# Optimization experiments

Measured on AMD Instinct MI355X. Metric: run time of the kernel, lower is better.

Reference implementation:

```python
import jax, jax.numpy as jnp
import numpy as np

IN_CH = 8      # in_channels
CIN = 80       # cin_channels (mel)
DI_BASE = 2
POS_GROUP = 4
NCH = 256      # n_channels
NLAYERS = 8
K = 3          # kernel_size
B = 1          # spect batch; audio batch = B * POS_GROUP
T = 4096
C2L = 2 * NCH * NLAYERS


def _conv1x1(x, w, b):
    # x: [B, C, T], w: [O, C], b: [O]
    return jnp.einsum('bct,oc->bot', x, w) + b[None, :, None]


def _dilated_conv(x, w, b, dilation):
    # x: [B, C, T], w: [O, C, K], 'same' padding as in torch Conv1d
    pad = dilation * (K - 1) // 2
    y = jax.lax.conv_general_dilated(
        x, w, window_strides=(1,), padding=[(pad, pad)],
        rhs_dilation=(dilation,), dimension_numbers=('NCH', 'OIH', 'NCH'))
    return y + b[None, :, None]


def setup_inputs() -> dict:
    key = jax.random.key(0)
    ks = jax.random.split(key, 12)
    s = 0.05
    d = {}
    d['audio'] = jax.random.normal(ks[0], (B * POS_GROUP, IN_CH, T), jnp.float32)
    d['spect'] = jax.random.normal(ks[1], (B, CIN, T), jnp.float32)
    d['pos'] = jax.random.randint(ks[2], (B * POS_GROUP,), 0, POS_GROUP)
    d['start_w'] = jax.random.normal(ks[3], (NCH, IN_CH), jnp.float32) * s
    d['start_b'] = jnp.zeros((NCH,), jnp.float32)
    d['cond_w'] = jax.random.normal(ks[4], (C2L, CIN), jnp.float32) * s
    d['cond_b'] = jnp.zeros((C2L,), jnp.float32)
    d['pos_emb_w'] = jax.random.normal(ks[5], (POS_GROUP, 128), jnp.float32) * s
    d['pos_lin_w'] = jax.random.normal(ks[6], (C2L, 128), jnp.float32) * s
    d['pos_lin_b'] = jnp.zeros((C2L,), jnp.float32)
    d['in_w'] = jax.random.normal(ks[7], (NLAYERS, 2 * NCH, NCH, K), jnp.float32) * s
    d['in_b'] = jnp.zeros((NLAYERS, 2 * NCH), jnp.float32)
    d['rs_w'] = jax.random.normal(ks[8], (NLAYERS - 1, 2 * NCH, NCH), jnp.float32) * s
    d['rs_b'] = jnp.zeros((NLAYERS - 1, 2 * NCH), jnp.float32)
    d['rs_last_w'] = jax.random.normal(ks[9], (NCH, NCH), jnp.float32) * s
    d['rs_last_b'] = jnp.zeros((NCH,), jnp.float32)
    d['end_w'] = jax.random.normal(ks[10], (2 * IN_CH, NCH), jnp.float32) * s
    d['end_b'] = jnp.zeros((2 * IN_CH,), jnp.float32)
    return d


def reference(audio, spect, pos, start_w, start_b, cond_w, cond_b,
              pos_emb_w, pos_lin_w, pos_lin_b, in_w, in_b,
              rs_w, rs_b, rs_last_w, rs_last_b, end_w, end_b):
    h = _conv1x1(audio, start_w, start_b)               # [BG, NCH, T]
    out = jnp.zeros_like(h)
    cond = _conv1x1(spect, cond_w, cond_b)              # [B, 2*NCH*L, T]
    # repeat(1, pos_group, 1).view(-1, C, T) == consecutive batch tiling
    cond = jnp.repeat(cond, POS_GROUP, axis=0)          # [BG, 2*NCH*L, T]
    pe = jax.nn.relu(pos_emb_w[pos])                    # [BG, 128]
    pc = (pe @ pos_lin_w.T + pos_lin_b)[:, :, None]     # [BG, 2*NCH*L, 1]
    for i in range(NLAYERS):
        off = i * 2 * NCH
        in_act = (_dilated_conv(h, in_w[i], in_b[i], DI_BASE ** i)
                  + cond[:, off:off + 2 * NCH]
                  + pc[:, off:off + 2 * NCH])
        acts = jnp.tanh(in_act[:, :NCH]) * jax.nn.sigmoid(in_act[:, NCH:])
        if i < NLAYERS - 1:
            rs = _conv1x1(acts, rs_w[i], rs_b[i])       # [BG, 2*NCH, T]
            h = h + rs[:, :NCH]
            out = out + rs[:, NCH:]
        else:
            out = out + _conv1x1(acts, rs_last_w, rs_last_b)
    y = _conv1x1(out, end_w, end_b)                     # [BG, 2*IN_CH, T]
    return y[:, :IN_CH], y[:, IN_CH:]
```

## Files before the change

kernel.cpp:

```cpp
#include <hip/hip_runtime.h>
#include <stdint.h>

#define T_LEN 4096
#define PAD   128
#define HROWS (T_LEN + 2*PAD)
#define NCH   256
#define M2    512
#define BG    4
#define NL    8

using f4  = __attribute__((ext_vector_type(4))) float;
using bh8 = __attribute__((ext_vector_type(8))) short;
using s4v = __attribute__((ext_vector_type(4))) short;
using u4  = __attribute__((ext_vector_type(4))) unsigned int;

static __device__ __forceinline__ short f2b(float f){
  unsigned u = __builtin_bit_cast(unsigned, f);
  unsigned r = (u + 0x7FFFu + ((u >> 16) & 1u)) >> 16;
  return (short)r;
}
static __device__ __forceinline__ float b2f(short s){
  unsigned u = ((unsigned)(unsigned short)s) << 16;
  return __builtin_bit_cast(float, u);
}

#define MFMA(a,b,c) __builtin_amdgcn_mfma_f32_16x16x32_bf16((a),(b),(c),0,0,0)


#define PAD_BLK0 1024
#define E_BLK0   1280
#define ST_BLK0  1408
#define CB_BLK0  1536
#define H0_BLK0  1600
#define ALL_BLKS 1856

__global__ __launch_bounds__(256) void prep_all(
    const float* __restrict__ audio, const float* __restrict__ spect,
    const int* __restrict__ pos, const float* __restrict__ start_w,
    const float* __restrict__ start_b, const float* __restrict__ cond_w,
    const float* __restrict__ cond_b, const float* __restrict__ pos_emb_w,
    const float* __restrict__ pos_lin_w, const float* __restrict__ pos_lin_b,
    const float* __restrict__ in_w, const float* __restrict__ in_b,
    const float* __restrict__ rs_w, const float* __restrict__ rs_b,
    const float* __restrict__ rs_last_w, const float* __restrict__ rs_last_b,
    const float* __restrict__ end_w, const float* __restrict__ end_b,
    short* __restrict__ W1, short* __restrict__ W2, short* __restrict__ Wcn,
    float* __restrict__ rsb8, short* __restrict__ hA, short* __restrict__ hB,
    short* __restrict__ Es, float* __restrict__ ebl, short* __restrict__ spectT,
    float* __restrict__ cb){
  __shared__ float smem[4224];
  const int bid = blockIdx.x, tid = threadIdx.x;

  if (bid < PAD_BLK0){
    const int n1 = NL*3*8*8*4*512;
    const int n2 = NL*8*8*2*512;
    const int n4 = NL*8*4*4*512;
    const int n3 = NL*M2;
    for (int i = bid*256 + tid; i < n1+n2+n4+n3; i += 1024*256){
      if (i < n1){
        int j = i & 7, lane = (i >> 3) & 63, f = (i >> 9) & 3, kk = (i >> 11) & 7, w = (i >> 14) & 7;
        int lt = i >> 17;
        int tap = lt % 3, l = lt / 3;
        int o = (f < 2) ? (w*32 + f*16 + (lane & 15)) : (256 + w*32 + (f-2)*16 + (lane & 15));
        int c = kk*32 + (lane >> 4)*8 + j;
        W1[i] = f2b(in_w[(((l*M2 + o)*NCH + c)*3) + tap]);
      } else if (i < n1+n2){
        int q = i - n1;
        int j = q & 7, lane = (q >> 3) & 63, f = (q >> 9) & 1, kk = (q >> 10) & 7, w = (q >> 13) & 7;
        int l = q >> 16;
        int o = w*32 + f*16 + (lane & 15);
        int c = kk*32 + (lane >> 4)*8 + j;
        W2[q] = (l < 7) ? f2b(rs_w[((size_t)(l*M2 + o))*NCH + c]) : (short)0;
      } else if (i < n1+n2+n4){
        int r = i - n1 - n2;
        int j = r & 7, lane = (r >> 3) & 63, f = (r >> 9) & 3, kk = (r >> 11) & 3, w = (r >> 13) & 7;
        int l = r >> 16;
        int o = (f < 2) ? (w*32 + f*16 + (lane & 15)) : (256 + w*32 + (f-2)*16 + (lane & 15));
        int k = kk*32 + (lane >> 4)*8 + j;
        Wcn[r] = (k < 80) ? f2b(cond_w[(size_t)(l*M2 + o)*80 + k]) : (short)0;
      } else {
        int k = i - n1 - n2 - n4;
        int o = k & 511, l = k >> 9;
        rsb8[k] = (l < 7) ? rs_b[l*M2 + o] : 0.f;
      }
    }
  } else if (bid < E_BLK0){
    int i = (bid - PAD_BLK0)*256 + tid;
    short* h = (i < 32768) ? hA : hB;
    int j = (i & 32767) << 3;
    int b = j >> 16;
    int r = j & 65535;
    int row = r >> 8, c = r & 255;
    int grow = (row < PAD) ? row : (T_LEN + PAD + (row - PAD));
    *(u4*)(h + ((size_t)b*HROWS + grow)*NCH + c) = (u4){0,0,0,0};
  } else if (bid < ST_BLK0){
    float* ew_s = smem; float* red = smem + 256;
    int e = bid - E_BLK0;
    const int l = e >> 4, o = e & 15;
    const int c = tid;
    ew_s[c] = end_w[o*256 + c];
    __syncthreads();
    const float* Wsrc = (l < 7) ? (rs_w + ((size_t)(l*M2 + NCH))*NCH) : rs_last_w;
    float acc = 0.f;
    #pragma unroll 8
    for (int cp = 0; cp < 256; ++cp)
      acc += ew_s[cp] * Wsrc[(size_t)cp*NCH + c];
    int kk = c >> 5, g = (c >> 3) & 3, j = c & 7;
    Es[(((size_t)l*8 + kk)*64 + g*16 + o)*8 + j] = f2b(acc);
    float bv = (l < 7) ? rs_b[l*M2 + NCH + c] : rs_last_b[c];
    red[c] = ew_s[c] * bv;
    __syncthreads();
    for (int s = 128; s > 0; s >>= 1){
      if (c < s) red[c] += red[c + s];
      __syncthreads();
    }
    if (c == 0) ebl[l*16 + o] = red[0] + ((l == 0) ? end_b[o] : 0.f);
  } else if (bid < CB_BLK0){
    float (*tile)[65] = (float(*)[65])smem;
    int e = bid - ST_BLK0;
    int t0 = (e & 63)*64, k0 = (e >> 6)*64;
    for (int i = tid; i < 64*64; i += 256){
      int kr = i >> 6, tt = i & 63;
      int k = k0 + kr;
      tile[kr][tt] = (k < 80) ? spect[(size_t)k*T_LEN + t0 + tt] : 0.f;
    }
    __syncthreads();
    for (int i = tid; i < 64*64; i += 256){
      int r = i >> 6, kk = i & 63;
      spectT[(size_t)(t0 + r)*128 + k0 + kk] = f2b(tile[kk][r]);
    }
  } else if (bid < H0_BLK0){
    int e = bid - CB_BLK0;
    int b = e >> 4;
    int ch = (e & 15)*256 + tid;
    int p = pos[b];
    float acc = pos_lin_b[ch] + in_b[ch] + cond_b[ch];
    for (int k = 0; k < 128; ++k){
      float ev = pos_emb_w[p*128 + k];
      ev = ev > 0.f ? ev : 0.f;
      acc += ev * pos_lin_w[ch*128 + k];
    }
    cb[b*4096 + ch] = acc;
  } else {
    float* sw = smem; float* sb = smem + 2048;
    int e = bid - H0_BLK0;
    int b = e >> 6, t0 = (e & 63)*64;
    for (int i = tid; i < NCH*8; i += 256) sw[i] = start_w[i];
    for (int i = tid; i < NCH;   i += 256) sb[i] = start_b[i];
    __syncthreads();
    int t = t0 + (tid & 63);
    int cg = tid >> 6;
    float av[8];
    #pragma unroll
    for (int ic = 0; ic < 8; ++ic) av[ic] = audio[((size_t)(b*8 + ic))*T_LEN + t];
    short* dst = hA + ((size_t)b*HROWS + PAD + t)*NCH;
    for (int c = cg*64; c < cg*64 + 64; ++c){
      float acc = sb[c];
      #pragma unroll
      for (int ic = 0; ic < 8; ++ic) acc += sw[c*8 + ic]*av[ic];
      dst[c] = f2b(acc);
    }
  }
}

__global__ __launch_bounds__(512, 2) void wn_layer(
    const short* __restrict__ hSrc, short* __restrict__ hDst,
    const short* __restrict__ W1l, const short* __restrict__ W2l,
    const short* __restrict__ Wcl, const short* __restrict__ Esl,
    const short* __restrict__ spectTp,
    const float* __restrict__ cb_l, const float* __restrict__ rsb_l,
    const float* __restrict__ ebl_l, float* __restrict__ yacc,
    int dil, int flags){

  __shared__ short Ht[3*64*NCH];
  __shared__ short xb[64*NCH];
  __shared__ short St[64*128];

  const int tid  = threadIdx.x;
  const int w    = tid >> 6, lane = tid & 63;
  const int l15  = lane & 15, g = lane >> 4;
  const int tile = blockIdx.x, b = blockIdx.y;
  const int sw8  = (l15 & 7) << 3;
  const bool first = flags & 1, last = flags & 2;

  f4 acc[4][4];
  #pragma unroll
  for (int f = 0; f < 4; ++f)
    #pragma unroll
    for (int nf = 0; nf < 4; ++nf) acc[f][nf] = (f4){0.f,0.f,0.f,0.f};

  bh8 Ap[3][4], Bp[3][4];

#define LAc(S, BUF) do{ const short* _p = Wcl + w*8192 + (S)*2048 + lane*8; \
    Ap[BUF][0]=*(const bh8*)(_p);      Ap[BUF][1]=*(const bh8*)(_p+512); \
    Ap[BUF][2]=*(const bh8*)(_p+1024); Ap[BUF][3]=*(const bh8*)(_p+1536); }while(0)
#define LBc(S, BUF) do{ const int _c=((S)*32+g*8)^sw8; \
    Bp[BUF][0]=*(const bh8*)(St + ( 0+l15)*128 + _c); \
    Bp[BUF][1]=*(const bh8*)(St + (16+l15)*128 + _c); \
    Bp[BUF][2]=*(const bh8*)(St + (32+l15)*128 + _c); \
    Bp[BUF][3]=*(const bh8*)(St + (48+l15)*128 + _c); }while(0)
#define LA1(S, BUF) do{ const int _tap=(S)>>3, _kk=(S)&7; \
    const short* _p = W1l + _tap*131072 + w*16384 + _kk*2048 + lane*8; \
    Ap[BUF][0]=*(const bh8*)(_p);      Ap[BUF][1]=*(const bh8*)(_p+512); \
    Ap[BUF][2]=*(const bh8*)(_p+1024); Ap[BUF][3]=*(const bh8*)(_p+1536); }while(0)
#define LB1(S, BUF) do{ const int _tap=(S)>>3, _kk=(S)&7; const int _c=(_kk*32+g*8)^sw8; \
    Bp[BUF][0]=*(const bh8*)(Ht + _tap*16384 + ( 0+l15)*NCH + _c); \
    Bp[BUF][1]=*(const bh8*)(Ht + _tap*16384 + (16+l15)*NCH + _c); \
    Bp[BUF][2]=*(const bh8*)(Ht + _tap*16384 + (32+l15)*NCH + _c); \
    Bp[BUF][3]=*(const bh8*)(Ht + _tap*16384 + (48+l15)*NCH + _c); }while(0)
#define LAX(S, BUF) do{ if((S)<3) LAc((S),BUF); else LA1((S)-3,BUF); }while(0)
#define LBX(S, BUF) do{ if((S)<3) LBc((S),BUF); else LB1((S)-3,BUF); }while(0)
#define LA2(S, BUF) do{ \
    const short* _p = W2l + w*8192 + (S)*1024 + lane*8; \
    Ap[BUF][0]=*(const bh8*)(_p);      Ap[BUF][1]=*(const bh8*)(_p+512); }while(0)
#define LB2(S, BUF) do{ const int _c=((S)*32+g*8)^sw8; \
    Bp[BUF][0]=*(const bh8*)(xb + ( 0+l15)*NCH + _c); \
    Bp[BUF][1]=*(const bh8*)(xb + (16+l15)*NCH + _c); \
    Bp[BUF][2]=*(const bh8*)(xb + (32+l15)*NCH + _c); \
    Bp[BUF][3]=*(const bh8*)(xb + (48+l15)*NCH + _c); }while(0)

  LAX(0, 0);

  {
    const int rsub = tid >> 5;
    const int innr = (tid & 31) << 3;
    #pragma unroll
    for (int tap = 0; tap < 3; ++tap){
      const int gbase = b*HROWS + PAD + tile*64 + (tap-1)*dil;
      #pragma unroll
      for (int ch = 0; ch < 4; ++ch){
        int r = ch*16 + rsub;
        u4 v = *(const u4*)(hSrc + (size_t)(gbase + r)*NCH + innr);
        *(u4*)(Ht + tap*16384 + r*NCH + (innr ^ ((r & 7) << 3))) = v;
      }
    }
    #pragma unroll
    for (int s = 0; s < 2; ++s){
      int id = tid + s*512;
      int r = id >> 4, c8 = (id & 15) << 3;
      u4 v = *(const u4*)(spectTp + (size_t)(tile*64 + r)*128 + c8);
      *(u4*)(St + r*128 + (c8 ^ ((r & 7) << 3))) = v;
    }
  }
  __syncthreads();

  LBX(0, 0);
  LAX(1, 1); LBX(1, 1);
  #pragma unroll
  for (int s = 0; s < 27; ++s){
    const int cur = s % 3, pf = (s+2) % 3;
    if (s < 25){ LAX(s+2, pf); LBX(s+2, pf); }
    #pragma unroll
    for (int f = 0; f < 4; ++f)
      #pragma unroll
      for (int nf = 0; nf < 4; ++nf)
        acc[f][nf] = MFMA(Ap[cur][f], Bp[cur][nf], acc[f][nf]);
  }

  float bias[4][4];
  #pragma unroll
  for (int f = 0; f < 4; ++f){
    int ch = ((f < 2) ? (w*32 + f*16) : (256 + w*32 + (f-2)*16)) + 4*g;
    f4 t = *(const f4*)(cb_l + b*4096 + ch);
    #pragma unroll
    for (int j = 0; j < 4; ++j) bias[f][j] = t[j];
  }
  float rbv[2][4];
  #pragma unroll
  for (int f = 0; f < 2; ++f){
    f4 t = *(const f4*)(rsb_l + w*32 + f*16 + 4*g);
    #pragma unroll
    for (int j = 0; j < 4; ++j) rbv[f][j] = t[j];
  }

  #pragma unroll
  for (int f = 0; f < 2; ++f){
    #pragma unroll
    for (int nf = 0; nf < 4; ++nf){
      int tl = nf*16 + l15;
      s4v pk;
      #pragma unroll
      for (int j = 0; j < 4; ++j){
        float xl = acc[f][nf][j]   + bias[f][j];
        float xh = acc[f+2][nf][j] + bias[f+2][j];
        xl = fminf(fmaxf(xl, -30.f), 30.f);
        xh = fminf(fmaxf(xh, -30.f), 30.f);
        float e2 = __expf(2.f*xl);
        float th = (e2 - 1.f)/(e2 + 1.f);
        float sg = 1.f/(1.f + __expf(-xh));
        pk[j] = f2b(th * sg);
      }
      *(s4v*)(xb + tl*NCH + ((w*32 + f*16 + 4*g) ^ sw8)) = pk;
    }
  }
  if (!last) LA2(0, 0);
  __syncthreads();

  if (!last){
    #pragma unroll
    for (int f = 0; f < 2; ++f)
      #pragma unroll
      for (int nf = 0; nf < 4; ++nf) acc[f][nf] = (f4){0.f,0.f,0.f,0.f};
    LB2(0, 0);
    #pragma unroll
    for (int s = 0; s < 8; ++s){
      const int cur = s & 1, nxt = cur ^ 1;
      if (s < 7){ LA2(s+1, nxt); LB2(s+1, nxt); }
      #pragma unroll
      for (int f = 0; f < 2; ++f)
        #pragma unroll
        for (int nf = 0; nf < 4; ++nf)
          acc[f][nf] = MFMA(Ap[cur][f], Bp[cur][nf], acc[f][nf]);
    }
    #pragma unroll
    for (int f = 0; f < 2; ++f){
      #pragma unroll
      for (int nf = 0; nf < 4; ++nf){
        int tl = nf*16 + l15;
        int cb0 = w*32 + f*16 + 4*g;
        s4v hold = *(const s4v*)(Ht + 16384 + tl*NCH + (cb0 ^ sw8));
        s4v pk;
        #pragma unroll
        for (int j = 0; j < 4; ++j)
          pk[j] = f2b(b2f(hold[j]) + acc[f][nf][j] + rbv[f][j]);
        *(s4v*)(hDst + ((size_t)b*HROWS + PAD + tile*64 + tl)*NCH + cb0) = pk;
      }
    }
  }
  {
    const int nfq = w & 3, kh = w >> 2;
    f4 ya = (f4){0.f,0.f,0.f,0.f};
    #pragma unroll
    for (int s = 0; s < 4; ++s){
      int kks = kh*4 + s;
      bh8 av = *(const bh8*)(Esl + ((size_t)kks*64 + lane)*8);
      bh8 bv = *(const bh8*)(xb + (nfq*16 + l15)*NCH + ((kks*32 + g*8) ^ sw8));
      ya = MFMA(av, bv, ya);
    }
    float* yp = yacc + (((size_t)(b*T_LEN + tile*64 + nfq*16 + l15))*2 + kh)*16 + g*4;
    f4 prev = first ? (f4){0.f,0.f,0.f,0.f} : *(const f4*)yp;
    f4 o;
    #pragma unroll
    for (int j = 0; j < 4; ++j)
      o[j] = prev[j] + ya[j] + ((kh == 0) ? ebl_l[g*4 + j] : 0.f);
    *(f4*)yp = o;
  }
#undef LAc
#undef LBc
#undef LA1
#undef LB1
#undef LAX
#undef LBX
#undef LA2
#undef LB2
}

__global__ void final_y(const float* __restrict__ yacc, float* __restrict__ y){
  __shared__ float tl[16][65];
  int b = blockIdx.y, t0 = blockIdx.x*64;
  int i = threadIdx.x;
  #pragma unroll
  for (int s = 0; s < 4; ++s){
    int idx = i + s*256;
    int t = idx >> 4, o = idx & 15;
    size_t base = ((size_t)(b*T_LEN + t0 + t))*32 + o;
    tl[o][t] = yacc[base] + yacc[base + 16];
  }
  __syncthreads();
  #pragma unroll
  for (int s = 0; s < 4; ++s){
    int idx = i + s*256;
    int o = idx >> 6, t = idx & 63;
    float v = tl[o][t];
    float* dst = (o < 8) ? (y + ((size_t)(b*8 + o))*T_LEN)
                         : (y + 131072 + ((size_t)(b*8 + o - 8))*T_LEN);
    dst[t0 + t] = v;
  }
}

extern "C" void kernel_launch(void* const* d_in, const int* in_sizes, int n_in,
                              void* d_out, int out_size, void* d_ws, size_t ws_size,
                              hipStream_t stream){
  const float* audio      = (const float*)d_in[0];
  const float* spect      = (const float*)d_in[1];
  const int*   pos        = (const int*)  d_in[2];
  const float* start_w    = (const float*)d_in[3];
  const float* start_b    = (const float*)d_in[4];
  const float* cond_w     = (const float*)d_in[5];
  const float* cond_b     = (const float*)d_in[6];
  const float* pos_emb_w  = (const float*)d_in[7];
  const float* pos_lin_w  = (const float*)d_in[8];
  const float* pos_lin_b  = (const float*)d_in[9];
  const float* in_w       = (const float*)d_in[10];
  const float* in_b       = (const float*)d_in[11];
  const float* rs_w       = (const float*)d_in[12];
  const float* rs_b       = (const float*)d_in[13];
  const float* rs_last_w  = (const float*)d_in[14];
  const float* rs_last_b  = (const float*)d_in[15];
  const float* end_w      = (const float*)d_in[16];
  const float* end_b      = (const float*)d_in[17];
  float* y = (float*)d_out;

  char* ws = (char*)d_ws;
  size_t off = 0;
  auto alloc = [&](size_t bytes) -> void* {
    void* p = ws + off;
    off += (bytes + 255) & ~(size_t)255;
    return p;
  };
  const size_t hBytes = (size_t)BG*HROWS*NCH*2;
  short* hA     = (short*)alloc(hBytes);
  short* hB     = (short*)alloc(hBytes);
  short* W1     = (short*)alloc((size_t)NL*3*8*8*4*512*2);
  short* W2     = (short*)alloc((size_t)NL*8*8*2*512*2);
  short* Wcn    = (short*)alloc((size_t)NL*8*4*4*512*2);
  float* rsb8   = (float*)alloc((size_t)NL*M2*4);
  float* cb     = (float*)alloc((size_t)BG*4096*4);
  short* spectT = (short*)alloc((size_t)4096*128*2);
  short* Es     = (short*)alloc((size_t)NL*8*64*8*2);
  float* ebl    = (float*)alloc((size_t)NL*16*4);
  float* yacc   = (float*)alloc((size_t)BG*T_LEN*2*16*4);
  if (off > ws_size) return;

  prep_all<<<ALL_BLKS, 256, 0, stream>>>(
      audio, spect, pos, start_w, start_b, cond_w, cond_b, pos_emb_w, pos_lin_w,
      pos_lin_b, in_w, in_b, rs_w, rs_b, rs_last_w, rs_last_b, end_w, end_b,
      W1, W2, Wcn, rsb8, hA, hB, Es, ebl, spectT, cb);

  for (int l = 0; l < NL; ++l){
    const short* hS = (l & 1) ? hB : hA;
    short*       hD = (l & 1) ? hA : hB;
    int flags = (l == 0 ? 1 : 0) | (l == NL-1 ? 2 : 0);
    wn_layer<<<dim3(64, BG), 512, 0, stream>>>(
        hS, hD,
        W1 + (size_t)l*3*131072,
        W2 + (size_t)l*65536,
        Wcn + (size_t)l*65536,
        Es + (size_t)l*4096,
        spectT,
        cb + l*M2,
        rsb8 + l*M2,
        ebl + l*16,
        yacc, 1 << l, flags);
  }
  final_y<<<dim3(64, BG), 256, 0, stream>>>(yacc, y);
}
```

Before: 219.6 us.

## Split wn_layer work across 16 waves with 1024-thread blocks

Each layer block now runs 16 waves instead of 8, and each wave owns 16 output channels (tanh and sigmoid halves) instead of 32. The weight pre-swizzle in prep_all, the register tiles, the prefetch pipeline, the residual GEMM and the end-projection partial sums (now four k-slices in yacc) are all re-laid out to match. The aim is more wave-level parallelism and latency hiding per CU, given only 256 blocks. In exchange the smaller per-wave tile means less operand reuse, and 1024-thread blocks allow at most one block per CU.

New measurement: 233.1 us. 6.2% more time.

```diff
diff --git a/kernel.cpp b/kernel.cpp
--- a/kernel.cpp
+++ b/kernel.cpp
@@ -52,30 +52,30 @@
   const int bid = blockIdx.x, tid = threadIdx.x;
 
   if (bid < PAD_BLK0){
-    const int n1 = NL*3*8*8*4*512;
-    const int n2 = NL*8*8*2*512;
-    const int n4 = NL*8*4*4*512;
+    const int n1 = NL*3*16*8*2*512;
+    const int n2 = NL*16*8*512;
+    const int n4 = NL*16*4*2*512;
     const int n3 = NL*M2;
     for (int i = bid*256 + tid; i < n1+n2+n4+n3; i += 1024*256){
       if (i < n1){
-        int j = i & 7, lane = (i >> 3) & 63, f = (i >> 9) & 3, kk = (i >> 11) & 7, w = (i >> 14) & 7;
+        int j = i & 7, lane = (i >> 3) & 63, f = (i >> 9) & 1, kk = (i >> 10) & 7, w = (i >> 13) & 15;
         int lt = i >> 17;
         int tap = lt % 3, l = lt / 3;
-        int o = (f < 2) ? (w*32 + f*16 + (lane & 15)) : (256 + w*32 + (f-2)*16 + (lane & 15));
+        int o = (f == 0) ? (w*16 + (lane & 15)) : (256 + w*16 + (lane & 15));
         int c = kk*32 + (lane >> 4)*8 + j;
         W1[i] = f2b(in_w[(((l*M2 + o)*NCH + c)*3) + tap]);
       } else if (i < n1+n2){
         int q = i - n1;
-        int j = q & 7, lane = (q >> 3) & 63, f = (q >> 9) & 1, kk = (q >> 10) & 7, w = (q >> 13) & 7;
+        int j = q & 7, lane = (q >> 3) & 63, kk = (q >> 9) & 7, w = (q >> 12) & 15;
         int l = q >> 16;
-        int o = w*32 + f*16 + (lane & 15);
+        int o = w*16 + (lane & 15);
         int c = kk*32 + (lane >> 4)*8 + j;
         W2[q] = (l < 7) ? f2b(rs_w[((size_t)(l*M2 + o))*NCH + c]) : (short)0;
       } else if (i < n1+n2+n4){
         int r = i - n1 - n2;
-        int j = r & 7, lane = (r >> 3) & 63, f = (r >> 9) & 3, kk = (r >> 11) & 3, w = (r >> 13) & 7;
+        int j = r & 7, lane = (r >> 3) & 63, f = (r >> 9) & 1, kk = (r >> 10) & 3, w = (r >> 12) & 15;
         int l = r >> 16;
-        int o = (f < 2) ? (w*32 + f*16 + (lane & 15)) : (256 + w*32 + (f-2)*16 + (lane & 15));
+        int o = (f == 0) ? (w*16 + (lane & 15)) : (256 + w*16 + (lane & 15));
         int k = kk*32 + (lane >> 4)*8 + j;
         Wcn[r] = (k < 80) ? f2b(cond_w[(size_t)(l*M2 + o)*80 + k]) : (short)0;
       } else {
@@ -163,7 +163,7 @@
   }
 }
 
-__global__ __launch_bounds__(512, 2) void wn_layer(
+__global__ __launch_bounds__(1024) void wn_layer(
     const short* __restrict__ hSrc, short* __restrict__ hDst,
     const short* __restrict__ W1l, const short* __restrict__ W2l,
     const short* __restrict__ Wcl, const short* __restrict__ Esl,
@@ -183,26 +183,24 @@
   const int sw8  = (l15 & 7) << 3;
   const bool first = flags & 1, last = flags & 2;
 
-  f4 acc[4][4];
-  #pragma unroll
-  for (int f = 0; f < 4; ++f)
+  f4 acc[2][4];
+  #pragma unroll
+  for (int f = 0; f < 2; ++f)
     #pragma unroll
     for (int nf = 0; nf < 4; ++nf) acc[f][nf] = (f4){0.f,0.f,0.f,0.f};
 
-  bh8 Ap[3][4], Bp[3][4];
-
-#define LAc(S, BUF) do{ const short* _p = Wcl + w*8192 + (S)*2048 + lane*8; \
-    Ap[BUF][0]=*(const bh8*)(_p);      Ap[BUF][1]=*(const bh8*)(_p+512); \
-    Ap[BUF][2]=*(const bh8*)(_p+1024); Ap[BUF][3]=*(const bh8*)(_p+1536); }while(0)
+  bh8 Ap[3][2], Bp[2][4];
+
+#define LAc(S, BUF) do{ const short* _p = Wcl + w*4096 + (S)*1024 + lane*8; \
+    Ap[BUF][0]=*(const bh8*)(_p); Ap[BUF][1]=*(const bh8*)(_p+512); }while(0)
 #define LBc(S, BUF) do{ const int _c=((S)*32+g*8)^sw8; \
     Bp[BUF][0]=*(const bh8*)(St + ( 0+l15)*128 + _c); \
     Bp[BUF][1]=*(const bh8*)(St + (16+l15)*128 + _c); \
     Bp[BUF][2]=*(const bh8*)(St + (32+l15)*128 + _c); \
     Bp[BUF][3]=*(const bh8*)(St + (48+l15)*128 + _c); }while(0)
 #define LA1(S, BUF) do{ const int _tap=(S)>>3, _kk=(S)&7; \
-    const short* _p = W1l + _tap*131072 + w*16384 + _kk*2048 + lane*8; \
-    Ap[BUF][0]=*(const bh8*)(_p);      Ap[BUF][1]=*(const bh8*)(_p+512); \
-    Ap[BUF][2]=*(const bh8*)(_p+1024); Ap[BUF][3]=*(const bh8*)(_p+1536); }while(0)
+    const short* _p = W1l + _tap*131072 + w*8192 + _kk*1024 + lane*8; \
+    Ap[BUF][0]=*(const bh8*)(_p); Ap[BUF][1]=*(const bh8*)(_p+512); }while(0)
 #define LB1(S, BUF) do{ const int _tap=(S)>>3, _kk=(S)&7; const int _c=(_kk*32+g*8)^sw8; \
     Bp[BUF][0]=*(const bh8*)(Ht + _tap*16384 + ( 0+l15)*NCH + _c); \
     Bp[BUF][1]=*(const bh8*)(Ht + _tap*16384 + (16+l15)*NCH + _c); \
@@ -211,8 +209,8 @@
 #define LAX(S, BUF) do{ if((S)<3) LAc((S),BUF); else LA1((S)-3,BUF); }while(0)
 #define LBX(S, BUF) do{ if((S)<3) LBc((S),BUF); else LB1((S)-3,BUF); }while(0)
 #define LA2(S, BUF) do{ \
-    const short* _p = W2l + w*8192 + (S)*1024 + lane*8; \
-    Ap[BUF][0]=*(const bh8*)(_p);      Ap[BUF][1]=*(const bh8*)(_p+512); }while(0)
+    const short* _p = W2l + w*4096 + (S)*512 + lane*8; \
+    Ap[BUF][0]=*(const bh8*)(_p); }while(0)
 #define LB2(S, BUF) do{ const int _c=((S)*32+g*8)^sw8; \
     Bp[BUF][0]=*(const bh8*)(xb + ( 0+l15)*NCH + _c); \
     Bp[BUF][1]=*(const bh8*)(xb + (16+l15)*NCH + _c); \
@@ -220,24 +218,22 @@
     Bp[BUF][3]=*(const bh8*)(xb + (48+l15)*NCH + _c); }while(0)
 
   LAX(0, 0);
+  LAX(1, 1);
 
   {
-    const int rsub = tid >> 5;
-    const int innr = (tid & 31) << 3;
     #pragma unroll
     for (int tap = 0; tap < 3; ++tap){
       const int gbase = b*HROWS + PAD + tile*64 + (tap-1)*dil;
       #pragma unroll
-      for (int ch = 0; ch < 4; ++ch){
-        int r = ch*16 + rsub;
+      for (int ch = 0; ch < 2; ++ch){
+        int id = tid + ch*1024;
+        int r = id >> 5, innr = (id & 31) << 3;
         u4 v = *(const u4*)(hSrc + (size_t)(gbase + r)*NCH + innr);
         *(u4*)(Ht + tap*16384 + r*NCH + (innr ^ ((r & 7) << 3))) = v;
       }
     }
-    #pragma unroll
-    for (int s = 0; s < 2; ++s){
-      int id = tid + s*512;
-      int r = id >> 4, c8 = (id & 15) << 3;
+    {
+      int r = tid >> 4, c8 = (tid & 15) << 3;
       u4 v = *(const u4*)(spectTp + (size_t)(tile*64 + r)*128 + c8);
       *(u4*)(St + r*128 + (c8 ^ ((r & 7) << 3))) = v;
     }
@@ -245,99 +241,87 @@
   __syncthreads();
 
   LBX(0, 0);
-  LAX(1, 1); LBX(1, 1);
   #pragma unroll
   for (int s = 0; s < 27; ++s){
-    const int cur = s % 3, pf = (s+2) % 3;
-    if (s < 25){ LAX(s+2, pf); LBX(s+2, pf); }
-    #pragma unroll
-    for (int f = 0; f < 4; ++f)
+    const int curA = s % 3, curB = s & 1;
+    if (s < 25) LAX(s+2, (s+2) % 3);
+    if (s < 26) LBX(s+1, curB ^ 1);
+    #pragma unroll
+    for (int f = 0; f < 2; ++f)
       #pragma unroll
       for (int nf = 0; nf < 4; ++nf)
-        acc[f][nf] = MFMA(Ap[cur][f], Bp[cur][nf], acc[f][nf]);
-  }
-
-  float bias[4][4];
-  #pragma unroll
-  for (int f = 0; f < 4; ++f){
-    int ch = ((f < 2) ? (w*32 + f*16) : (256 + w*32 + (f-2)*16)) + 4*g;
-    f4 t = *(const f4*)(cb_l + b*4096 + ch);
+        acc[f][nf] = MFMA(Ap[curA][f], Bp[curB][nf], acc[f][nf]);
+  }
+
+  float bias[2][4];
+  #pragma unroll
+  for (int f = 0; f < 2; ++f){
+    f4 t = *(const f4*)(cb_l + b*4096 + f*256 + w*16 + 4*g);
     #pragma unroll
     for (int j = 0; j < 4; ++j) bias[f][j] = t[j];
   }
-  float rbv[2][4];
-  #pragma unroll
-  for (int f = 0; f < 2; ++f){
-    f4 t = *(const f4*)(rsb_l + w*32 + f*16 + 4*g);
-    #pragma unroll
-    for (int j = 0; j < 4; ++j) rbv[f][j] = t[j];
-  }
-
-  #pragma unroll
-  for (int f = 0; f < 2; ++f){
-    #pragma unroll
-    for (int nf = 0; nf < 4; ++nf){
-      int tl = nf*16 + l15;
-      s4v pk;
-      #pragma unroll
-      for (int j = 0; j < 4; ++j){
-        float xl = acc[f][nf][j]   + bias[f][j];
-        float xh = acc[f+2][nf][j] + bias[f+2][j];
-        xl = fminf(fmaxf(xl, -30.f), 30.f);
-        xh = fminf(fmaxf(xh, -30.f), 30.f);
-        float e2 = __expf(2.f*xl);
-        float th = (e2 - 1.f)/(e2 + 1.f);
-        float sg = 1.f/(1.f + __expf(-xh));
-        pk[j] = f2b(th * sg);
-      }
-      *(s4v*)(xb + tl*NCH + ((w*32 + f*16 + 4*g) ^ sw8)) = pk;
-    }
+  float rbv[4];
+  {
+    f4 t = *(const f4*)(rsb_l + w*16 + 4*g);
+    #pragma unroll
+    for (int j = 0; j < 4; ++j) rbv[j] = t[j];
+  }
+
+  #pragma unroll
+  for (int nf = 0; nf < 4; ++nf){
+    int tl = nf*16 + l15;
+    s4v pk;
+    #pragma unroll
+    for (int j = 0; j < 4; ++j){
+      float xl = acc[0][nf][j] + bias[0][j];
+      float xh = acc[1][nf][j] + bias[1][j];
+      xl = fminf(fmaxf(xl, -30.f), 30.f);
+      xh = fminf(fmaxf(xh, -30.f), 30.f);
+      float e2 = __expf(2.f*xl);
+      float th = (e2 - 1.f)/(e2 + 1.f);
+      float sg = 1.f/(1.f + __expf(-xh));
+      pk[j] = f2b(th * sg);
+    }
+    *(s4v*)(xb + tl*NCH + ((w*16 + 4*g) ^ sw8)) = pk;
   }
   if (!last) LA2(0, 0);
   __syncthreads();
 
   if (!last){
     #pragma unroll
-    for (int f = 0; f < 2; ++f)
-      #pragma unroll
-      for (int nf = 0; nf < 4; ++nf) acc[f][nf] = (f4){0.f,0.f,0.f,0.f};
+    for (int nf = 0; nf < 4; ++nf) acc[0][nf] = (f4){0.f,0.f,0.f,0.f};
     LB2(0, 0);
     #pragma unroll
     for (int s = 0; s < 8; ++s){
       const int cur = s & 1, nxt = cur ^ 1;
       if (s < 7){ LA2(s+1, nxt); LB2(s+1, nxt); }
       #pragma unroll
-      for (int f = 0; f < 2; ++f)
-        #pragma unroll
-        for (int nf = 0; nf < 4; ++nf)
-          acc[f][nf] = MFMA(Ap[cur][f], Bp[cur][nf], acc[f][nf]);
-    }
-    #pragma unroll
-    for (int f = 0; f < 2; ++f){
+      for (int nf = 0; nf < 4; ++nf)
+        acc[0][nf] = MFMA(Ap[cur][0], Bp[cur][nf], acc[0][nf]);
+    }
+    #pragma unroll
+    for (int nf = 0; nf < 4; ++nf){
+      int tl = nf*16 + l15;
+      int cb0 = w*16 + 4*g;
+      s4v hold = *(const s4v*)(Ht + 16384 + tl*NCH + (cb0 ^ sw8));
+      s4v pk;
       #pragma unroll
-      for (int nf = 0; nf < 4; ++nf){
-        int tl = nf*16 + l15;
-        int cb0 = w*32 + f*16 + 4*g;
-        s4v hold = *(const s4v*)(Ht + 16384 + tl*NCH + (cb0 ^ sw8));
-        s4v pk;
-        #pragma unroll
-        for (int j = 0; j < 4; ++j)
-          pk[j] = f2b(b2f(hold[j]) + acc[f][nf][j] + rbv[f][j]);
-        *(s4v*)(hDst + ((size_t)b*HROWS + PAD + tile*64 + tl)*NCH + cb0) = pk;
-      }
+      for (int j = 0; j < 4; ++j)
+        pk[j] = f2b(b2f(hold[j]) + acc[0][nf][j] + rbv[j]);
+      *(s4v*)(hDst + ((size_t)b*HROWS + PAD + tile*64 + tl)*NCH + cb0) = pk;
     }
   }
   {
     const int nfq = w & 3, kh = w >> 2;
     f4 ya = (f4){0.f,0.f,0.f,0.f};
     #pragma unroll
-    for (int s = 0; s < 4; ++s){
-      int kks = kh*4 + s;
+    for (int s = 0; s < 2; ++s){
+      int kks = kh*2 + s;
       bh8 av = *(const bh8*)(Esl + ((size_t)kks*64 + lane)*8);
       bh8 bv = *(const bh8*)(xb + (nfq*16 + l15)*NCH + ((kks*32 + g*8) ^ sw8));
       ya = MFMA(av, bv, ya);
     }
-    float* yp = yacc + (((size_t)(b*T_LEN + tile*64 + nfq*16 + l15))*2 + kh)*16 + g*4;
+    float* yp = yacc + (((size_t)(b*T_LEN + tile*64 + nfq*16 + l15))*4 + kh)*16 + g*4;
     f4 prev = first ? (f4){0.f,0.f,0.f,0.f} : *(const f4*)yp;
     f4 o;
     #pragma unroll
@@ -363,8 +347,8 @@
   for (int s = 0; s < 4; ++s){
     int idx = i + s*256;
     int t = idx >> 4, o = idx & 15;
-    size_t base = ((size_t)(b*T_LEN + t0 + t))*32 + o;
-    tl[o][t] = yacc[base] + yacc[base + 16];
+    size_t base = ((size_t)(b*T_LEN + t0 + t))*64 + o;
+    tl[o][t] = yacc[base] + yacc[base + 16] + yacc[base + 32] + yacc[base + 48];
   }
   __syncthreads();
   #pragma unroll
@@ -411,15 +395,15 @@
   const size_t hBytes = (size_t)BG*HROWS*NCH*2;
   short* hA     = (short*)alloc(hBytes);
   short* hB     = (short*)alloc(hBytes);
-  short* W1     = (short*)alloc((size_t)NL*3*8*8*4*512*2);
-  short* W2     = (short*)alloc((size_t)NL*8*8*2*512*2);
-  short* Wcn    = (short*)alloc((size_t)NL*8*4*4*512*2);
+  short* W1     = (short*)alloc((size_t)NL*3*16*8*2*512*2);
+  short* W2     = (short*)alloc((size_t)NL*16*8*512*2);
+  short* Wcn    = (short*)alloc((size_t)NL*16*4*2*512*2);
   float* rsb8   = (float*)alloc((size_t)NL*M2*4);
   float* cb     = (float*)alloc((size_t)BG*4096*4);
   short* spectT = (short*)alloc((size_t)4096*128*2);
   short* Es     = (short*)alloc((size_t)NL*8*64*8*2);
   float* ebl    = (float*)alloc((size_t)NL*16*4);
-  float* yacc   = (float*)alloc((size_t)BG*T_LEN*2*16*4);
+  float* yacc   = (float*)alloc((size_t)BG*T_LEN*4*16*4);
   if (off > ws_size) return;
 
   prep_all<<<ALL_BLKS, 256, 0, stream>>>(
@@ -431,7 +415,7 @@
     const short* hS = (l & 1) ? hB : hA;
     short*       hD = (l & 1) ? hA : hB;
     int flags = (l == 0 ? 1 : 0) | (l == NL-1 ? 2 : 0);
-    wn_layer<<<dim3(64, BG), 512, 0, stream>>>(
+    wn_layer<<<dim3(64, BG), 1024, 0, stream>>>(
         hS, hD,
         W1 + (size_t)l*3*131072,
         W2 + (size_t)l*65536,
```

## Vectorize weight packing, dedupe dilated-conv halo loads, remap block order

Applied to the files above, without the earlier changes.

The prep kernel now packs eight bf16 weights per thread with vector loads and one 16-byte store, instead of converting and storing one short per thread. The layer kernel loads the overlapping dilated-conv window once, as 64+2*dil contiguous rows when dil<=64, rather than three separate 64-row tap copies. Tap operands and the residual read are then addressed by row offset into that shared buffer. Block indices are also permuted so concurrently running blocks touch different tiles and batches, which is meant to change cache locality. The cost is more complex indexing and a special path for the largest dilation.

Measured after the change: 220.2 us, median of 2. Within noise of the previous version (+0.2%).

```diff
diff --git a/kernel.cpp b/kernel.cpp
--- a/kernel.cpp
+++ b/kernel.cpp
@@ -52,34 +52,58 @@
   const int bid = blockIdx.x, tid = threadIdx.x;
 
   if (bid < PAD_BLK0){
-    const int n1 = NL*3*8*8*4*512;
-    const int n2 = NL*8*8*2*512;
-    const int n4 = NL*8*4*4*512;
+    const int G1 = NL*3*8*8*4*64;
+    const int G2 = NL*8*8*2*64;
+    const int G4 = NL*8*4*4*64;
     const int n3 = NL*M2;
-    for (int i = bid*256 + tid; i < n1+n2+n4+n3; i += 1024*256){
-      if (i < n1){
-        int j = i & 7, lane = (i >> 3) & 63, f = (i >> 9) & 3, kk = (i >> 11) & 7, w = (i >> 14) & 7;
-        int lt = i >> 17;
+    for (int q = bid*256 + tid; q < G1+G2+G4+n3; q += 1024*256){
+      if (q < G1){
+        int lane = q & 63, f = (q >> 6) & 3, kk = (q >> 8) & 7, w = (q >> 11) & 7;
+        int lt = q >> 14;
         int tap = lt % 3, l = lt / 3;
         int o = (f < 2) ? (w*32 + f*16 + (lane & 15)) : (256 + w*32 + (f-2)*16 + (lane & 15));
-        int c = kk*32 + (lane >> 4)*8 + j;
-        W1[i] = f2b(in_w[(((l*M2 + o)*NCH + c)*3) + tap]);
-      } else if (i < n1+n2){
-        int q = i - n1;
-        int j = q & 7, lane = (q >> 3) & 63, f = (q >> 9) & 1, kk = (q >> 10) & 7, w = (q >> 13) & 7;
-        int l = q >> 16;
+        int c0 = kk*32 + (lane >> 4)*8;
+        const float* src = in_w + (((size_t)(l*M2 + o)*NCH + c0)*3) + tap;
+        bh8 pk;
+        #pragma unroll
+        for (int j = 0; j < 8; ++j) pk[j] = f2b(src[j*3]);
+        *(bh8*)(W1 + (size_t)q*8) = pk;
+      } else if (q < G1+G2){
+        int p = q - G1;
+        int lane = p & 63, f = (p >> 6) & 1, kk = (p >> 7) & 7, w = (p >> 10) & 7;
+        int l = p >> 13;
         int o = w*32 + f*16 + (lane & 15);
-        int c = kk*32 + (lane >> 4)*8 + j;
-        W2[q] = (l < 7) ? f2b(rs_w[((size_t)(l*M2 + o))*NCH + c]) : (short)0;
-      } else if (i < n1+n2+n4){
-        int r = i - n1 - n2;
-        int j = r & 7, lane = (r >> 3) & 63, f = (r >> 9) & 3, kk = (r >> 11) & 3, w = (r >> 13) & 7;
-        int l = r >> 16;
+        int c0 = kk*32 + (lane >> 4)*8;
+        bh8 pk;
+        if (l < 7){
+          const f4* s = (const f4*)(rs_w + ((size_t)(l*M2 + o))*NCH + c0);
+          f4 a = s[0], bvv = s[1];
+          #pragma unroll
+          for (int j = 0; j < 4; ++j){ pk[j] = f2b(a[j]); pk[4+j] = f2b(bvv[j]); }
+        } else {
+          #pragma unroll
+          for (int j = 0; j < 8; ++j) pk[j] = 0;
+        }
+        *(bh8*)(W2 + (size_t)p*8) = pk;
+      } else if (q < G1+G2+G4){
+        int p = q - G1 - G2;
+        int lane = p & 63, f = (p >> 6) & 3, kk = (p >> 8) & 3, w = (p >> 10) & 7;
+        int l = p >> 13;
         int o = (f < 2) ? (w*32 + f*16 + (lane & 15)) : (256 + w*32 + (f-2)*16 + (lane & 15));
-        int k = kk*32 + (lane >> 4)*8 + j;
-        Wcn[r] = (k < 80) ? f2b(cond_w[(size_t)(l*M2 + o)*80 + k]) : (short)0;
+        int k0 = kk*32 + (lane >> 4)*8;
+        bh8 pk;
+        if (k0 < 80){
+          const f4* s = (const f4*)(cond_w + (size_t)(l*M2 + o)*80 + k0);
+          f4 a = s[0], bvv = s[1];
+          #pragma unroll
+          for (int j = 0; j < 4; ++j){ pk[j] = f2b(a[j]); pk[4+j] = f2b(bvv[j]); }
+        } else {
+          #pragma unroll
+          for (int j = 0; j < 8; ++j) pk[j] = 0;
+        }
+        *(bh8*)(Wcn + (size_t)p*8) = pk;
       } else {
-        int k = i - n1 - n2 - n4;
+        int k = q - G1 - G2 - G4;
         int o = k & 511, l = k >> 9;
         rsb8[k] = (l < 7) ? rs_b[l*M2 + o] : 0.f;
       }
@@ -172,16 +196,19 @@
     const float* __restrict__ ebl_l, float* __restrict__ yacc,
     int dil, int flags){
 
-  __shared__ short Ht[3*64*NCH];
+  __shared__ short Ht[192*NCH];
   __shared__ short xb[64*NCH];
   __shared__ short St[64*128];
 
   const int tid  = threadIdx.x;
   const int w    = tid >> 6, lane = tid & 63;
   const int l15  = lane & 15, g = lane >> 4;
-  const int tile = blockIdx.x, b = blockIdx.y;
+  const int lin  = blockIdx.x + (blockIdx.y << 6);
+  const int nl2  = ((lin & 7) << 5) + (lin >> 3);
+  const int tile = nl2 & 63, b = nl2 >> 6;
   const int sw8  = (l15 & 7) << 3;
   const bool first = flags & 1, last = flags & 2;
+  const int tbR  = (dil <= 64) ? dil : 64;
 
   f4 acc[4][4];
   #pragma unroll
@@ -203,11 +230,13 @@
     const short* _p = W1l + _tap*131072 + w*16384 + _kk*2048 + lane*8; \
     Ap[BUF][0]=*(const bh8*)(_p);      Ap[BUF][1]=*(const bh8*)(_p+512); \
     Ap[BUF][2]=*(const bh8*)(_p+1024); Ap[BUF][3]=*(const bh8*)(_p+1536); }while(0)
-#define LB1(S, BUF) do{ const int _tap=(S)>>3, _kk=(S)&7; const int _c=(_kk*32+g*8)^sw8; \
-    Bp[BUF][0]=*(const bh8*)(Ht + _tap*16384 + ( 0+l15)*NCH + _c); \
-    Bp[BUF][1]=*(const bh8*)(Ht + _tap*16384 + (16+l15)*NCH + _c); \
-    Bp[BUF][2]=*(const bh8*)(Ht + _tap*16384 + (32+l15)*NCH + _c); \
-    Bp[BUF][3]=*(const bh8*)(Ht + _tap*16384 + (48+l15)*NCH + _c); }while(0)
+#define LB1(S, BUF) do{ const int _tap=(S)>>3, _kk=(S)&7; \
+    const int _tb=_tap*tbR; const int _sw=(((_tb+l15)&7)<<3); \
+    const short* _hb = Ht + (_tb+l15)*NCH + ((_kk*32+g*8)^_sw); \
+    Bp[BUF][0]=*(const bh8*)(_hb); \
+    Bp[BUF][1]=*(const bh8*)(_hb + 16*NCH); \
+    Bp[BUF][2]=*(const bh8*)(_hb + 32*NCH); \
+    Bp[BUF][3]=*(const bh8*)(_hb + 48*NCH); }while(0)
 #define LAX(S, BUF) do{ if((S)<3) LAc((S),BUF); else LA1((S)-3,BUF); }while(0)
 #define LBX(S, BUF) do{ if((S)<3) LBc((S),BUF); else LB1((S)-3,BUF); }while(0)
 #define LA2(S, BUF) do{ \
@@ -222,17 +251,13 @@
   LAX(0, 0);
 
   {
-    const int rsub = tid >> 5;
-    const int innr = (tid & 31) << 3;
-    #pragma unroll
-    for (int tap = 0; tap < 3; ++tap){
-      const int gbase = b*HROWS + PAD + tile*64 + (tap-1)*dil;
-      #pragma unroll
-      for (int ch = 0; ch < 4; ++ch){
-        int r = ch*16 + rsub;
-        u4 v = *(const u4*)(hSrc + (size_t)(gbase + r)*NCH + innr);
-        *(u4*)(Ht + tap*16384 + r*NCH + (innr ^ ((r & 7) << 3))) = v;
-      }
+    const int nrows32 = ((dil <= 64) ? (64 + 2*dil) : 192) * 32;
+    for (int i = tid; i < nrows32; i += 512){
+      int r = i >> 5, c16 = (i & 31) << 3;
+      int grow = (dil <= 64) ? (tile*64 - dil + r)
+                             : (tile*64 + ((r >> 6) - 1)*128 + (r & 63));
+      u4 v = *(const u4*)(hSrc + ((size_t)(b*HROWS + PAD + grow))*NCH + c16);
+      *(u4*)(Ht + r*NCH + (c16 ^ ((r & 7) << 3))) = v;
     }
     #pragma unroll
     for (int s = 0; s < 2; ++s){
@@ -312,13 +337,14 @@
         for (int nf = 0; nf < 4; ++nf)
           acc[f][nf] = MFMA(Ap[cur][f], Bp[cur][nf], acc[f][nf]);
     }
+    const int swc = (((tbR + l15) & 7) << 3);
     #pragma unroll
     for (int f = 0; f < 2; ++f){
       #pragma unroll
       for (int nf = 0; nf < 4; ++nf){
         int tl = nf*16 + l15;
         int cb0 = w*32 + f*16 + 4*g;
-        s4v hold = *(const s4v*)(Ht + 16384 + tl*NCH + (cb0 ^ sw8));
+        s4v hold = *(const s4v*)(Ht + (tbR + tl)*NCH + (cb0 ^ swc));
         s4v pk;
         #pragma unroll
         for (int j = 0; j < 4; ++j)
```
